# Kernel tuning notes

Measured on AMD Instinct MI355X. Metric: run time of the kernel, lower is better.

Reference implementation:

```python
import jax, jax.numpy as jnp
import numpy as np

MAX_LAB = 64  # cap on connected-component ids per sample (original cc3d is unbounded)
BIG = jnp.int32(2 ** 30)


def _cc_label(mask):
    """26-connectivity connected components of a 3D bool mask via label propagation.
    Each component ends with label == max initial voxel id in it (nonzero), bg = 0."""
    n = mask.size
    init = jnp.where(mask, jnp.arange(1, n + 1, dtype=jnp.int32).reshape(mask.shape), jnp.int32(0))

    def cond(st):
        return jnp.any(st[0] != st[1])

    def body(st):
        lab = st[0]
        # max over 3x3x3 neighborhood == 26-connectivity propagation step
        neigh = jax.lax.reduce_window(lab, jnp.int32(0), jax.lax.max, (3, 3, 3), (1, 1, 1), 'SAME')
        return (jnp.where(mask, neigh, jnp.int32(0)), lab)

    lab, _ = jax.lax.while_loop(cond, body, (init, jnp.full_like(init, -1)))
    return lab


def _compact(lab):
    """Relabel a per-sample label map to consecutive ids 0,1..k (0 = background),
    matching cc3d's 1..k numbering."""
    u = jnp.unique(lab, size=MAX_LAB + 1, fill_value=BIG)  # sorted: [0, l1, .., lk, BIG..]
    return jnp.searchsorted(u, lab).astype(jnp.int32)


def _instance_dice(x, y):
    xb = jnp.squeeze(x, 1) > 0.5  # [B,D,H,W] pred foreground
    yb = jnp.squeeze(y, 1) > 0.5  # [B,D,H,W] gt foreground
    label = jax.vmap(lambda m: _compact(_cc_label(m)))
    gt_lab = label(yb)  # per-sample ids 0..k_i (ids shared across batch, as in original)
    pr_lab = label(xb)
    M = MAX_LAB + 1
    # joint histogram over (gt component id, pred component id), global across batch
    idx = gt_lab.reshape(-1) * M + pr_lab.reshape(-1)
    overlap = jax.ops.segment_sum(jnp.ones(idx.shape, jnp.float32), idx, num_segments=M * M).reshape(M, M)
    gt_size = overlap.sum(1)  # [M] voxels per gt id
    pr_size = overlap.sum(0)  # [M] voxels per pred id
    ov = overlap[1:, 1:]                       # [G,P] fg-fg overlaps
    inter_mask = ov > 0                        # pred comp p intersects gt comp g
    inter = ov.sum(1)                          # [G] |gt_g  ∩  union(intersecting preds)|
    union_sz = (inter_mask * pr_size[1:]).sum(1)  # [G] |union of intersecting pred comps|
    has_inter = inter > 0
    dice = jnp.where(has_inter, 2.0 * inter / jnp.maximum(union_sz + gt_size[1:], 1.0), 0.0)
    lesion_dice = dice.sum()
    num_gt = jnp.sum(gt_size[1:] > 0).astype(jnp.float32)
    tp_mask = inter_mask.any(0)                # [P] pred comps matched to some gt
    num_fp = jnp.sum((pr_size[1:] > 0) & ~tp_mask).astype(jnp.float32)
    return lesion_dice / (num_gt + num_fp)


def setup_inputs() -> dict:
    B, D, H, W = 2, 128, 128, 128
    R, N_BLOBS = 5, 12
    rng = np.random.default_rng(0)
    zz, yy, xx = np.meshgrid(np.arange(D), np.arange(H), np.arange(W), indexing='ij')

    def blobs(k):
        m = np.zeros((B, D, H, W), bool)
        for b in range(B):
            c = rng.integers(R + 2, D - R - 2, size=(k, 3))
            for cz, cy, cx in c:
                m[b] |= (zz - cz) ** 2 + (yy - cy) ** 2 + (xx - cx) ** 2 <= R * R
        return m

    y = blobs(N_BLOBS)
    # prediction = slightly shifted gt (partial-overlap TPs) + extra false-positive blobs
    x = np.roll(y, shift=(2, 1, 0), axis=(1, 2, 3)) | blobs(4)
    return {"x": jnp.asarray(x[:, None].astype(np.float32)),
            "y": jnp.asarray(y[:, None].astype(np.float32))}


def reference(x, y):
    return _instance_dice(x, y)
```

## Files before the change

kernel.cpp:

```cpp
#include <hip/hip_runtime.h>


#define NVOX (128 * 128 * 128)
#define NTOT (2 * NVOX)
#define NBLK 4096
#define CAP 12288
#define ML 65
#define NSLAB 8
#define ZSLAB 16

__global__ __launch_bounds__(256) void k_count(
    const float4* __restrict__ x, const float4* __restrict__ y,
    unsigned char* __restrict__ maskArr, int* __restrict__ blkCnt,
    int* __restrict__ overlap) {
    int t = blockIdx.x * 256 + threadIdx.x;
    float4 xv = x[t];
    float4 yv = y[t];
    unsigned m = 0;
    if (xv.x > 0.5f) m |= 1u;
    if (xv.y > 0.5f) m |= 2u;
    if (xv.z > 0.5f) m |= 4u;
    if (xv.w > 0.5f) m |= 8u;
    if (yv.x > 0.5f) m |= 16u;
    if (yv.y > 0.5f) m |= 32u;
    if (yv.z > 0.5f) m |= 64u;
    if (yv.w > 0.5f) m |= 128u;
    maskArr[t] = (unsigned char)m;
    int v = __popc(m & 0xFu) | (__popc(m >> 4) << 16);
    #pragma unroll
    for (int d = 1; d < 64; d <<= 1) v += __shfl_xor(v, d);
    __shared__ int ws[4];
    if ((threadIdx.x & 63) == 0) ws[threadIdx.x >> 6] = v;
    __syncthreads();
    if (threadIdx.x == 0) blkCnt[blockIdx.x] = ws[0] + ws[1] + ws[2] + ws[3];
    if (blockIdx.x == 0)
        for (int i = threadIdx.x; i < ML * ML; i += 256) overlap[i] = 0;
}

__global__ __launch_bounds__(1024) void k_scan(
    const int* __restrict__ blkCnt, int* __restrict__ blkOff, int* __restrict__ cnt) {
    int t = threadIdx.x;
    int base = t * 4;
    int a0 = blkCnt[base], a1 = blkCnt[base + 1], a2 = blkCnt[base + 2], a3 = blkCnt[base + 3];
    int s = a0 + a1 + a2 + a3;
    int lane = t & 63, wave = t >> 6;
    int v = s;
    #pragma unroll
    for (int d = 1; d < 64; d <<= 1) {
        int u = __shfl_up(v, d);
        if (lane >= d) v += u;
    }
    __shared__ int wsum[16];
    __shared__ int segb;
    if (lane == 63) wsum[wave] = v;
    __syncthreads();
    int woff = 0;
    for (int k = 0; k < wave; ++k) woff += wsum[k];
    int incl = v + woff;
    int excl = incl - s;
    if (t == 511) segb = incl;
    __syncthreads();
    int sub = (base >= 2048) ? segb : 0;
    int e0 = excl - sub;
    blkOff[base]     = e0;
    blkOff[base + 1] = e0 + a0;
    blkOff[base + 2] = e0 + a0 + a1;
    blkOff[base + 3] = e0 + a0 + a1 + a2;
    if (t == 511) { cnt[0] = incl & 0xFFFF; cnt[2] = incl >> 16; }
    if (t == 1023) {
        cnt[1] = (incl & 0xFFFF) - (segb & 0xFFFF);
        cnt[3] = (incl >> 16)    - (segb >> 16);
    }
}

__global__ __launch_bounds__(256) void k_fill(
    const unsigned char* __restrict__ maskArr, const int* __restrict__ blkOff,
    unsigned short* __restrict__ posMapX, unsigned short* __restrict__ posMapY,
    int* __restrict__ lists) {
    int blk = blockIdx.x;
    int t = blk * 256 + threadIdx.x;
    int b = blk >> 11;
    unsigned m = maskArr[t];
    int px = __popc(m & 0xFu), py = __popc(m >> 4);
    int pk = px | (py << 16);
    int lane = threadIdx.x & 63, wave = threadIdx.x >> 6;
    int v = pk;
    #pragma unroll
    for (int d = 1; d < 64; d <<= 1) {
        int u = __shfl_up(v, d);
        if (lane >= d) v += u;
    }
    __shared__ int wsum[4];
    if (lane == 63) wsum[wave] = v;
    __syncthreads();
    int woff = 0;
    for (int k = 0; k < wave; ++k) woff += wsum[k];
    int incl = v + woff;
    int off = blkOff[blk];
    int baseX = (off & 0xFFFF) + (incl & 0xFFFF) - px;
    int baseY = (off >> 16)    + (incl >> 16)    - py;
    int i = t << 2;
    int j = i & (NVOX - 1);
    ushort4 pxv, pyv;
    unsigned short* ppx = &pxv.x;
    unsigned short* ppy = &pyv.x;
    int cx = 0, cy = 0;
    #pragma unroll
    for (int k = 0; k < 4; ++k) {
        unsigned short vx = 0, vy = 0;
        if (m & (1u << k)) {
            int pos = baseX + cx++;
            if (pos < CAP) { lists[(0 + b) * CAP + pos] = j + k; vx = (unsigned short)(pos + 1); }
        }
        if (m & (1u << (k + 4))) {
            int pos = baseY + cy++;
            if (pos < CAP) { lists[(2 + b) * CAP + pos] = j + k; vy = (unsigned short)(pos + 1); }
        }
        ppx[k] = vx;
        ppy[k] = vy;
    }
    ((ushort4*)posMapX)[t] = pxv;
    ((ushort4*)posMapY)[t] = pyv;
}

__device__ __forceinline__ int find_root(volatile unsigned* parent, int i) {
    unsigned p = parent[i];
    while (p != (unsigned)i) {
        unsigned gp = parent[p];
        if (gp != p) parent[i] = gp;
        i = (int)p;
        p = gp;
    }
    return i;
}

__device__ __forceinline__ void lds_union(unsigned* parentNV, int a, int b) {
    volatile unsigned* parent = (volatile unsigned*)parentNV;
    int ra = find_root(parent, a);
    int rb = find_root(parent, b);
    while (ra != rb) {
        int lo = ra < rb ? ra : rb;
        int hi = ra < rb ? rb : ra;
        unsigned old = atomicCAS(&parentNV[lo], (unsigned)lo, (unsigned)hi);
        if (old == (unsigned)lo) return;
        ra = find_root(parent, (int)old);
        rb = find_root(parent, hi);
    }
}

__global__ __launch_bounds__(1024) void k_cc_local(
    const unsigned short* __restrict__ posMapX, const unsigned short* __restrict__ posMapY,
    const int* __restrict__ lists, const int* __restrict__ blkOff,
    const int* __restrict__ cnt, int* __restrict__ rootPos) {
    int fb = blockIdx.y;
    int slab = blockIdx.x;
    int f = fb >> 1, b = fb & 1;
    const unsigned short* posMap = (f ? posMapY : posMapX) + (b << 21);
    const int* fgl = lists + fb * CAP;
    int n = cnt[fb]; if (n > CAP) n = CAP;
    int blkbase = b * 2048 + slab * 256;
    int o0 = blkOff[blkbase];
    int s0 = f ? (o0 >> 16) : (o0 & 0xFFFF);
    int s1;
    if (slab == NSLAB - 1) s1 = n;
    else { int o1 = blkOff[blkbase + 256]; s1 = f ? (o1 >> 16) : (o1 & 0xFFFF); }
    if (s1 > n) s1 = n;
    int ns = s1 - s0;
    if (ns <= 0) return;

    __shared__ unsigned parent[CAP];
    int tid = threadIdx.x;

    for (int q = tid; q < ns; q += 1024) {
        int p = s0 + q;
        int j = fgl[p];
        unsigned par = (unsigned)q;
        if (p + 1 < s1 && (j & 127) != 127) {
            if (fgl[p + 1] == j + 1) par = (unsigned)(q + 1);
        }
        parent[q] = par;
    }
    __syncthreads();

    for (int q = tid; q < ns; q += 1024) {
        int j = fgl[s0 + q];
        int z = j >> 14, y = (j >> 7) & 127, x0 = j & 127;
        bool ztop = ((z & (ZSLAB - 1)) == (ZSLAB - 1));
        unsigned short qv[12];
        int idx = 0;
        #pragma unroll
        for (int dx = -1; dx <= 1; ++dx) {
            int yy = y + 1, xx = x0 + dx;
            bool ok = yy <= 127 && (unsigned)xx <= 127u;
            int nj = (z << 14) + (yy << 7) + xx;
            qv[idx++] = ok ? posMap[nj] : (unsigned short)0;
        }
        #pragma unroll
        for (int dy = -1; dy <= 1; ++dy)
            #pragma unroll
            for (int dx = -1; dx <= 1; ++dx) {
                int zz = z + 1, yy = y + dy, xx = x0 + dx;
                bool ok = !ztop && zz <= 127 && (unsigned)yy <= 127u && (unsigned)xx <= 127u;
                int nj = (zz << 14) + (yy << 7) + xx;
                qv[idx++] = ok ? posMap[nj] : (unsigned short)0;
            }
        #pragma unroll
        for (int k = 0; k < 12; ++k)
            if (qv[k]) lds_union(parent, q, (int)qv[k] - 1 - s0);
    }
    __syncthreads();

    for (int q = tid; q < ns; q += 1024)
        rootPos[fb * CAP + s0 + q] = s0 + find_root((volatile unsigned*)parent, q);
}

__device__ __forceinline__ int rank_of(const int* sortedL, int nr, int v) {
    int lo = 0, hi = nr;
    while (lo < hi) { int mid = (lo + hi) >> 1; if (sortedL[mid] < v) lo = mid + 1; else hi = mid; }
    return lo;
}

__device__ __forceinline__ void hist_add(int* ovl, int key) {
    unsigned long long remaining = __ballot(1);
    int lane = threadIdx.x & 63;
    while (remaining) {
        int leader = __ffsll(remaining) - 1;
        int lkey = __shfl(key, leader);
        unsigned long long m = __ballot(lkey == key ? 1 : 0) & remaining;
        if (lane == leader) atomicAdd(&ovl[lkey], (int)__popcll(m));
        remaining &= ~m;
    }
}

__global__ __launch_bounds__(1024) void k_cc_merge(
    const unsigned short* __restrict__ posMapX, const unsigned short* __restrict__ posMapY,
    const int* __restrict__ lists, const int* __restrict__ cnt,
    const int* __restrict__ rootPos, int* __restrict__ overlap) {
    int b = blockIdx.x;
    int tid = threadIdx.x;
    int nX = cnt[b];     if (nX > CAP) nX = CAP;
    int nY = cnt[2 + b]; if (nY > CAP) nY = CAP;

    __shared__ unsigned par[2][CAP];
    __shared__ int sortedL[2][64];
    __shared__ int rootsL[128];
    __shared__ int nrA[2];
    __shared__ int ovl[ML * ML];

    for (int p = tid; p < nX; p += 1024) par[0][p] = (unsigned)rootPos[b * CAP + p];
    for (int p = tid; p < nY; p += 1024) par[1][p] = (unsigned)rootPos[(2 + b) * CAP + p];
    for (int i = tid; i < ML * ML; i += 1024) ovl[i] = 0;
    if (tid < 2) nrA[tid] = 0;
    __syncthreads();

    for (int f = 0; f < 2; ++f) {
        const unsigned short* pm = (f ? posMapY : posMapX) + (b << 21);
        const int* fgl = lists + (f * 2 + b) * CAP;
        int n = f ? nY : nX;
        unsigned* P = par[f];
        for (int p = tid; p < n; p += 1024) {
            int j = fgl[p];
            int z = j >> 14;
            if ((z & (ZSLAB - 1)) != (ZSLAB - 1) || z == 127) continue;
            int y = (j >> 7) & 127, x0 = j & 127;
            int zz = z + 1;
            unsigned short qv[9];
            int idx = 0;
            #pragma unroll
            for (int dy = -1; dy <= 1; ++dy)
                #pragma unroll
                for (int dx = -1; dx <= 1; ++dx) {
                    int yy = y + dy, xx = x0 + dx;
                    bool ok = (unsigned)yy <= 127u && (unsigned)xx <= 127u;
                    int nj = (zz << 14) + (yy << 7) + xx;
                    qv[idx++] = ok ? pm[nj] : (unsigned short)0;
                }
            #pragma unroll
            for (int k = 0; k < 9; ++k)
                if (qv[k]) lds_union(P, p, (int)qv[k] - 1);
        }
    }
    __syncthreads();

    for (int f = 0; f < 2; ++f) {
        int n = f ? nY : nX;
        unsigned* P = par[f];
        for (int p = tid; p < n; p += 1024)
            if (P[p] == (unsigned)p) {
                int s = atomicAdd(&nrA[f], 1);
                if (s < 128) rootsL[s] = p;
            }
        __syncthreads();
        int nr = nrA[f]; if (nr > 64) nr = 64;
        if (tid < nr) {
            int v = rootsL[tid];
            int r = 0;
            for (int k = 0; k < nr; ++k) r += (rootsL[k] < v) ? 1 : 0;
            sortedL[f][r] = v;
        }
        __syncthreads();
    }
    int nr0 = nrA[0]; if (nr0 > 64) nr0 = 64;
    int nr1 = nrA[1]; if (nr1 > 64) nr1 = 64;

    {
        const int* fglX = lists + (0 + b) * CAP;
        for (int t = tid; t < nX; t += 1024) {
            int j = fglX[t];
            int rX = find_root((volatile unsigned*)par[0], t);
            int pc = 1 + rank_of(sortedL[0], nr0, rX);
            int q = (int)posMapY[(b << 21) + j];
            int gc = 0;
            if (q) {
                int rY = find_root((volatile unsigned*)par[1], q - 1);
                gc = 1 + rank_of(sortedL[1], nr1, rY);
            }
            hist_add(ovl, gc * ML + pc);
        }
        const int* fglY = lists + (2 + b) * CAP;
        for (int t = tid; t < nY; t += 1024) {
            int j = fglY[t];
            if (posMapX[(b << 21) + j]) continue;
            int rY = find_root((volatile unsigned*)par[1], t);
            int gc = 1 + rank_of(sortedL[1], nr1, rY);
            hist_add(ovl, gc * ML);
        }
    }
    __syncthreads();
    for (int i = tid; i < ML * ML; i += 1024) {
        int v = ovl[i];
        if (v) atomicAdd(&overlap[i], v);
    }
}

__global__ void k_final(const int* __restrict__ overlap, float* __restrict__ out) {
    __shared__ int O[ML * ML];
    __shared__ float prs[ML];
    __shared__ unsigned char tp[ML];
    __shared__ float diceSh[ML];
    __shared__ int ngSh[ML];
    __shared__ int nfSh[ML];
    int tid = threadIdx.x;
    for (int i = tid; i < ML * ML; i += blockDim.x) O[i] = overlap[i];
    __syncthreads();
    if (tid < ML) {
        int s = 0; int any = 0;
        for (int g = 0; g < ML; ++g) {
            int o = O[g * ML + tid];
            s += o;
            if (g >= 1 && o > 0) any = 1;
        }
        prs[tid] = (float)s;
        tp[tid] = (unsigned char)any;
    }
    __syncthreads();
    if (tid < ML) {
        float dice = 0.f; int ng = 0, nf = 0;
        if (tid >= 1) {
            int gt = 0, inter = 0; float un = 0.f;
            for (int p = 0; p < ML; ++p) {
                int o = O[tid * ML + p];
                gt += o;
                if (p >= 1) { inter += o; if (o > 0) un += prs[p]; }
            }
            if (inter > 0) {
                float den = un + (float)gt;
                if (den < 1.f) den = 1.f;
                dice = 2.f * (float)inter / den;
            }
            ng = (gt > 0) ? 1 : 0;
            nf = (prs[tid] > 0.f && tp[tid] == 0) ? 1 : 0;
        }
        diceSh[tid] = dice; ngSh[tid] = ng; nfSh[tid] = nf;
    }
    __syncthreads();
    if (tid == 0) {
        float ld = 0.f; int ng = 0, nf = 0;
        for (int k = 1; k < ML; ++k) { ld += diceSh[k]; ng += ngSh[k]; nf += nfSh[k]; }
        out[0] = ld / (float)(ng + nf);
    }
}

extern "C" void kernel_launch(void* const* d_in, const int* in_sizes, int n_in,
                              void* d_out, int out_size, void* d_ws, size_t ws_size,
                              hipStream_t stream) {
    const float* x = (const float*)d_in[0];
    const float* y = (const float*)d_in[1];
    float* out = (float*)d_out;

    char* base = (char*)d_ws;
    int* cnt            = (int*)base;
    int* overlap        = cnt + 16;
    int* blkCnt         = overlap + ML * ML;
    int* blkOff         = blkCnt + NBLK;
    int* lists          = blkOff + NBLK;
    int* rootPos        = lists + 4 * CAP;
    unsigned char* maskArr = (unsigned char*)(rootPos + 4 * CAP);
    size_t off = (size_t)((maskArr + NTOT / 4) - (unsigned char*)base);
    off = (off + 15) & ~(size_t)15;
    unsigned short* posMapX = (unsigned short*)(base + off);
    unsigned short* posMapY = posMapX + NTOT;

    k_count<<<NBLK, 256, 0, stream>>>((const float4*)x, (const float4*)y,
                                      maskArr, blkCnt, overlap);
    k_scan<<<1, 1024, 0, stream>>>(blkCnt, blkOff, cnt);
    k_fill<<<NBLK, 256, 0, stream>>>(maskArr, blkOff, posMapX, posMapY, lists);
    k_cc_local<<<dim3(NSLAB, 4), 1024, 0, stream>>>(posMapX, posMapY, lists, blkOff, cnt, rootPos);
    k_cc_merge<<<2, 1024, 0, stream>>>(posMapX, posMapY, lists, cnt, rootPos, overlap);
    k_final<<<1, 256, 0, stream>>>(overlap, out);
}
```

Before: 172.5 us.

## Emit cross-slab edges from local CC and split merge into per-label and overlap kernels

The local connected-component pass now records edges that cross slab boundaries into a compacted global edge list, using a wave prefix-sum and one atomic per wave. The merge kernel then runs one block per field/batch and only unions those edges, then assigns compact labels to the slab roots. A separate, widely parallel kernel builds the overlap histogram with global atomics, replacing the two-block serial histogram pass. This adds a launch and global atomics on a small histogram, and drops edges silently if more than EDGE_CAP are produced.

```diff
diff --git a/kernel.cpp b/kernel.cpp
--- a/kernel.cpp
+++ b/kernel.cpp
@@ -8,11 +8,12 @@
 #define ML 65
 #define NSLAB 8
 #define ZSLAB 16
+#define EDGE_CAP 8192
 
 __global__ __launch_bounds__(256) void k_count(
     const float4* __restrict__ x, const float4* __restrict__ y,
     unsigned char* __restrict__ maskArr, int* __restrict__ blkCnt,
-    int* __restrict__ overlap) {
+    int* __restrict__ overlap, int* __restrict__ cnt) {
     int t = blockIdx.x * 256 + threadIdx.x;
     float4 xv = x[t];
     float4 yv = y[t];
@@ -33,8 +34,10 @@
     if ((threadIdx.x & 63) == 0) ws[threadIdx.x >> 6] = v;
     __syncthreads();
     if (threadIdx.x == 0) blkCnt[blockIdx.x] = ws[0] + ws[1] + ws[2] + ws[3];
-    if (blockIdx.x == 0)
+    if (blockIdx.x == 0) {
         for (int i = threadIdx.x; i < ML * ML; i += 256) overlap[i] = 0;
+        if (threadIdx.x < 8) cnt[8 + threadIdx.x] = 0;
+    }
 }
 
 __global__ __launch_bounds__(1024) void k_scan(
@@ -151,7 +154,7 @@
 __global__ __launch_bounds__(1024) void k_cc_local(
     const unsigned short* __restrict__ posMapX, const unsigned short* __restrict__ posMapY,
     const int* __restrict__ lists, const int* __restrict__ blkOff,
-    const int* __restrict__ cnt, int* __restrict__ rootPos) {
+    int* __restrict__ cnt, int* __restrict__ rootPos, int* __restrict__ edges) {
     int fb = blockIdx.y;
     int slab = blockIdx.x;
     int f = fb >> 1, b = fb & 1;
@@ -170,20 +173,27 @@
 
     __shared__ unsigned parent[CAP];
     int tid = threadIdx.x;
-
-    for (int q = tid; q < ns; q += 1024) {
-        int p = s0 + q;
-        int j = fgl[p];
-        unsigned par = (unsigned)q;
-        if (p + 1 < s1 && (j & 127) != 127) {
-            if (fgl[p + 1] == j + 1) par = (unsigned)(q + 1);
-        }
-        parent[q] = par;
-    }
-    __syncthreads();
-
-    for (int q = tid; q < ns; q += 1024) {
-        int j = fgl[s0 + q];
+    int lane = tid & 63;
+    int iters = (ns + 1023) >> 10;
+
+    for (int it = 0; it < iters; ++it) {
+        int q = it * 1024 + tid;
+        if (q < ns) {
+            int p = s0 + q;
+            int j = fgl[p];
+            unsigned par = (unsigned)q;
+            if (p + 1 < s1 && (j & 127) != 127) {
+                if (fgl[p + 1] == j + 1) par = (unsigned)(q + 1);
+            }
+            parent[q] = par;
+        }
+    }
+    __syncthreads();
+
+    for (int it = 0; it < iters; ++it) {
+        int q = it * 1024 + tid;
+        bool active = q < ns;
+        int j = active ? fgl[s0 + q] : 0;
         int z = j >> 14, y = (j >> 7) & 127, x0 = j & 127;
         bool ztop = ((z & (ZSLAB - 1)) == (ZSLAB - 1));
         unsigned short qv[12];
@@ -191,7 +201,7 @@
         #pragma unroll
         for (int dx = -1; dx <= 1; ++dx) {
             int yy = y + 1, xx = x0 + dx;
-            bool ok = yy <= 127 && (unsigned)xx <= 127u;
+            bool ok = active && yy <= 127 && (unsigned)xx <= 127u;
             int nj = (z << 14) + (yy << 7) + xx;
             qv[idx++] = ok ? posMap[nj] : (unsigned short)0;
         }
@@ -200,18 +210,48 @@
             #pragma unroll
             for (int dx = -1; dx <= 1; ++dx) {
                 int zz = z + 1, yy = y + dy, xx = x0 + dx;
-                bool ok = !ztop && zz <= 127 && (unsigned)yy <= 127u && (unsigned)xx <= 127u;
+                bool ok = active && zz <= 127 && (unsigned)yy <= 127u && (unsigned)xx <= 127u;
                 int nj = (zz << 14) + (yy << 7) + xx;
                 qv[idx++] = ok ? posMap[nj] : (unsigned short)0;
             }
         #pragma unroll
-        for (int k = 0; k < 12; ++k)
+        for (int k = 0; k < 3; ++k)
             if (qv[k]) lds_union(parent, q, (int)qv[k] - 1 - s0);
-    }
-    __syncthreads();
-
-    for (int q = tid; q < ns; q += 1024)
-        rootPos[fb * CAP + s0 + q] = s0 + find_root((volatile unsigned*)parent, q);
+        if (!ztop) {
+            #pragma unroll
+            for (int k = 3; k < 12; ++k)
+                if (qv[k]) lds_union(parent, q, (int)qv[k] - 1 - s0);
+        }
+        int ec = 0;
+        int myE[9];
+        if (ztop) {
+            #pragma unroll
+            for (int k = 3; k < 12; ++k)
+                if (qv[k]) myE[ec++] = (s0 + q) | (((int)qv[k] - 1) << 14);
+        }
+        int pref = ec;
+        #pragma unroll
+        for (int d = 1; d < 64; d <<= 1) {
+            int u = __shfl_up(pref, d);
+            if (lane >= d) pref += u;
+        }
+        int total = __shfl(pref, 63);
+        if (total > 0) {
+            int base = 0;
+            if (lane == 63) base = atomicAdd(cnt + 8 + fb, total);
+            base = __shfl(base, 63);
+            int o = base + pref - ec;
+            for (int k = 0; k < ec; ++k)
+                if (o + k < EDGE_CAP) edges[fb * EDGE_CAP + o + k] = myE[k];
+        }
+    }
+    __syncthreads();
+
+    for (int it = 0; it < iters; ++it) {
+        int q = it * 1024 + tid;
+        if (q < ns)
+            rootPos[fb * CAP + s0 + q] = s0 + find_root((volatile unsigned*)parent, q);
+    }
 }
 
 __device__ __forceinline__ int rank_of(const int* sortedL, int nr, int v) {
@@ -220,116 +260,95 @@
     return lo;
 }
 
-__device__ __forceinline__ void hist_add(int* ovl, int key) {
+__global__ __launch_bounds__(1024) void k_cc_merge(
+    const int* __restrict__ cnt, const int* __restrict__ rootPos,
+    const int* __restrict__ edges, unsigned char* __restrict__ lab8) {
+    int fb = blockIdx.x;
+    int tid = threadIdx.x;
+    int n = cnt[fb]; if (n > CAP) n = CAP;
+    int ne = cnt[8 + fb]; if (ne > EDGE_CAP) ne = EDGE_CAP;
+
+    __shared__ unsigned parent[CAP];
+    __shared__ int slabRoots[1024];
+    __shared__ int rootsL[128];
+    __shared__ int sortedL[64];
+    __shared__ int nsrSh, nrSh;
+
+    if (tid == 0) { nsrSh = 0; nrSh = 0; }
+    __syncthreads();
+    for (int p = tid; p < n; p += 1024) {
+        unsigned r = (unsigned)rootPos[fb * CAP + p];
+        parent[p] = r;
+        if (r == (unsigned)p) {
+            int s = atomicAdd(&nsrSh, 1);
+            if (s < 1024) slabRoots[s] = p;
+        }
+    }
+    __syncthreads();
+
+    for (int e = tid; e < ne; e += 1024) {
+        int pk = edges[fb * EDGE_CAP + e];
+        lds_union(parent, pk & 0x3FFF, pk >> 14);
+    }
+    __syncthreads();
+
+    int nsr = nsrSh; if (nsr > 1024) nsr = 1024;
+    for (int i = tid; i < nsr; i += 1024) {
+        int r = slabRoots[i];
+        if (parent[r] == (unsigned)r) {
+            int s = atomicAdd(&nrSh, 1);
+            if (s < 128) rootsL[s] = r;
+        }
+    }
+    __syncthreads();
+    int nr = nrSh; if (nr > 64) nr = 64;
+    if (tid < nr) {
+        int v = rootsL[tid];
+        int r = 0;
+        for (int k = 0; k < nr; ++k) r += (rootsL[k] < v) ? 1 : 0;
+        sortedL[r] = v;
+    }
+    __syncthreads();
+
+    for (int i = tid; i < nsr; i += 1024) {
+        int r = slabRoots[i];
+        int fr = find_root((volatile unsigned*)parent, r);
+        lab8[fb * CAP + r] = (unsigned char)(1 + rank_of(sortedL, nr, fr));
+    }
+}
+
+__global__ __launch_bounds__(256) void k_overlap(
+    const unsigned short* __restrict__ posMapX, const unsigned short* __restrict__ posMapY,
+    const int* __restrict__ lists, const int* __restrict__ cnt,
+    const int* __restrict__ rootPos, const unsigned char* __restrict__ lab8,
+    int* __restrict__ overlap) {
+    int fb = blockIdx.y;
+    int f = fb >> 1, b = fb & 1;
+    int n = cnt[fb]; if (n > CAP) n = CAP;
+    int t = blockIdx.x * blockDim.x + threadIdx.x;
+    if (t >= n) return;
+    int j = lists[fb * CAP + t];
+    int gi = (b << 21) + j;
+    int key;
+    if (f == 0) {
+        int pc = (int)lab8[fb * CAP + rootPos[fb * CAP + t]];
+        int q = (int)posMapY[gi];
+        int gc = 0;
+        if (q) gc = (int)lab8[(2 + b) * CAP + rootPos[(2 + b) * CAP + (q - 1)]];
+        key = gc * ML + pc;
+    } else {
+        if (posMapX[gi] != 0) return;
+        int gc = (int)lab8[fb * CAP + rootPos[fb * CAP + t]];
+        key = gc * ML;
+    }
     unsigned long long remaining = __ballot(1);
     int lane = threadIdx.x & 63;
     while (remaining) {
         int leader = __ffsll(remaining) - 1;
         int lkey = __shfl(key, leader);
         unsigned long long m = __ballot(lkey == key ? 1 : 0) & remaining;
-        if (lane == leader) atomicAdd(&ovl[lkey], (int)__popcll(m));
+        if (lane == leader) atomicAdd(&overlap[lkey], (int)__popcll(m));
         remaining &= ~m;
-    }
-}
-
-__global__ __launch_bounds__(1024) void k_cc_merge(
-    const unsigned short* __restrict__ posMapX, const unsigned short* __restrict__ posMapY,
-    const int* __restrict__ lists, const int* __restrict__ cnt,
-    const int* __restrict__ rootPos, int* __restrict__ overlap) {
-    int b = blockIdx.x;
-    int tid = threadIdx.x;
-    int nX = cnt[b];     if (nX > CAP) nX = CAP;
-    int nY = cnt[2 + b]; if (nY > CAP) nY = CAP;
-
-    __shared__ unsigned par[2][CAP];
-    __shared__ int sortedL[2][64];
-    __shared__ int rootsL[128];
-    __shared__ int nrA[2];
-    __shared__ int ovl[ML * ML];
-
-    for (int p = tid; p < nX; p += 1024) par[0][p] = (unsigned)rootPos[b * CAP + p];
-    for (int p = tid; p < nY; p += 1024) par[1][p] = (unsigned)rootPos[(2 + b) * CAP + p];
-    for (int i = tid; i < ML * ML; i += 1024) ovl[i] = 0;
-    if (tid < 2) nrA[tid] = 0;
-    __syncthreads();
-
-    for (int f = 0; f < 2; ++f) {
-        const unsigned short* pm = (f ? posMapY : posMapX) + (b << 21);
-        const int* fgl = lists + (f * 2 + b) * CAP;
-        int n = f ? nY : nX;
-        unsigned* P = par[f];
-        for (int p = tid; p < n; p += 1024) {
-            int j = fgl[p];
-            int z = j >> 14;
-            if ((z & (ZSLAB - 1)) != (ZSLAB - 1) || z == 127) continue;
-            int y = (j >> 7) & 127, x0 = j & 127;
-            int zz = z + 1;
-            unsigned short qv[9];
-            int idx = 0;
-            #pragma unroll
-            for (int dy = -1; dy <= 1; ++dy)
-                #pragma unroll
-                for (int dx = -1; dx <= 1; ++dx) {
-                    int yy = y + dy, xx = x0 + dx;
-                    bool ok = (unsigned)yy <= 127u && (unsigned)xx <= 127u;
-                    int nj = (zz << 14) + (yy << 7) + xx;
-                    qv[idx++] = ok ? pm[nj] : (unsigned short)0;
-                }
-            #pragma unroll
-            for (int k = 0; k < 9; ++k)
-                if (qv[k]) lds_union(P, p, (int)qv[k] - 1);
-        }
-    }
-    __syncthreads();
-
-    for (int f = 0; f < 2; ++f) {
-        int n = f ? nY : nX;
-        unsigned* P = par[f];
-        for (int p = tid; p < n; p += 1024)
-            if (P[p] == (unsigned)p) {
-                int s = atomicAdd(&nrA[f], 1);
-                if (s < 128) rootsL[s] = p;
-            }
-        __syncthreads();
-        int nr = nrA[f]; if (nr > 64) nr = 64;
-        if (tid < nr) {
-            int v = rootsL[tid];
-            int r = 0;
-            for (int k = 0; k < nr; ++k) r += (rootsL[k] < v) ? 1 : 0;
-            sortedL[f][r] = v;
-        }
-        __syncthreads();
-    }
-    int nr0 = nrA[0]; if (nr0 > 64) nr0 = 64;
-    int nr1 = nrA[1]; if (nr1 > 64) nr1 = 64;
-
-    {
-        const int* fglX = lists + (0 + b) * CAP;
-        for (int t = tid; t < nX; t += 1024) {
-            int j = fglX[t];
-            int rX = find_root((volatile unsigned*)par[0], t);
-            int pc = 1 + rank_of(sortedL[0], nr0, rX);
-            int q = (int)posMapY[(b << 21) + j];
-            int gc = 0;
-            if (q) {
-                int rY = find_root((volatile unsigned*)par[1], q - 1);
-                gc = 1 + rank_of(sortedL[1], nr1, rY);
-            }
-            hist_add(ovl, gc * ML + pc);
-        }
-        const int* fglY = lists + (2 + b) * CAP;
-        for (int t = tid; t < nY; t += 1024) {
-            int j = fglY[t];
-            if (posMapX[(b << 21) + j]) continue;
-            int rY = find_root((volatile unsigned*)par[1], t);
-            int gc = 1 + rank_of(sortedL[1], nr1, rY);
-            hist_add(ovl, gc * ML);
-        }
-    }
-    __syncthreads();
-    for (int i = tid; i < ML * ML; i += 1024) {
-        int v = ovl[i];
-        if (v) atomicAdd(&overlap[i], v);
     }
 }
 
@@ -395,17 +414,22 @@
     int* blkOff         = blkCnt + NBLK;
     int* lists          = blkOff + NBLK;
     int* rootPos        = lists + 4 * CAP;
-    unsigned char* maskArr = (unsigned char*)(rootPos + 4 * CAP);
+    int* edges          = rootPos + 4 * CAP;
+    unsigned char* lab8 = (unsigned char*)(edges + 4 * EDGE_CAP);
+    unsigned char* maskArr = lab8 + 4 * CAP;
     size_t off = (size_t)((maskArr + NTOT / 4) - (unsigned char*)base);
     off = (off + 15) & ~(size_t)15;
     unsigned short* posMapX = (unsigned short*)(base + off);
     unsigned short* posMapY = posMapX + NTOT;
 
     k_count<<<NBLK, 256, 0, stream>>>((const float4*)x, (const float4*)y,
-                                      maskArr, blkCnt, overlap);
+                                      maskArr, blkCnt, overlap, cnt);
     k_scan<<<1, 1024, 0, stream>>>(blkCnt, blkOff, cnt);
     k_fill<<<NBLK, 256, 0, stream>>>(maskArr, blkOff, posMapX, posMapY, lists);
-    k_cc_local<<<dim3(NSLAB, 4), 1024, 0, stream>>>(posMapX, posMapY, lists, blkOff, cnt, rootPos);
-    k_cc_merge<<<2, 1024, 0, stream>>>(posMapX, posMapY, lists, cnt, rootPos, overlap);
+    k_cc_local<<<dim3(NSLAB, 4), 1024, 0, stream>>>(posMapX, posMapY, lists,
+                                                    blkOff, cnt, rootPos, edges);
+    k_cc_merge<<<4, 1024, 0, stream>>>(cnt, rootPos, edges, lab8);
+    k_overlap<<<dim3((CAP + 255) / 256, 4), 256, 0, stream>>>(
+        posMapX, posMapY, lists, cnt, rootPos, lab8, overlap);
     k_final<<<1, 256, 0, stream>>>(overlap, out);
 }
```

Measured after the change: 145.2 us. -15.8%, faster.
